# Kernel optimization log

Hardware: AMD Instinct MI355X
Metric: run time of the kernel (lower is better)

## Reference

```python
import jax, jax.numpy as jnp
import numpy as np

NUM_EXPERTS = 8
DIM = 1024
HIDDEN = 2048
N_TOKENS = 8192  # rows of x, includes padding beyond sum(num_tokens_per_expert)


def setup_inputs() -> dict:
    key = jax.random.key(0)
    k_x, k_w1, k_w2, k_w3 = jax.random.split(key, 4)
    x = jax.random.normal(k_x, (N_TOKENS, DIM), dtype=jnp.float32)
    # trunc_normal(std=0.02)-like init; w2 is zeros in torch init but we use
    w1 = jax.random.normal(k_w1, (NUM_EXPERTS, HIDDEN, DIM), dtype=jnp.float32) * 0.02
    w2 = jax.random.normal(k_w2, (NUM_EXPERTS, DIM, HIDDEN), dtype=jnp.float32) * 0.02
    w3 = jax.random.normal(k_w3, (NUM_EXPERTS, HIDDEN, DIM), dtype=jnp.float32) * 0.02
    # routed token counts per expert; sum <= N_TOKENS, remainder is padding
    num_tokens_per_expert = jnp.array([995, 1000, 980, 1010, 970, 1020, 990, 1005], dtype=jnp.int64)
    return {"x": x, "num_tokens_per_expert": num_tokens_per_expert,
            "w1": w1, "w2": w2, "w3": w3}


def reference(x, num_tokens_per_expert, w1, w2, w3):
    # Mirrors torch _run_experts_for_loop with act='silu'. The torch code calls
    # .tolist() on the counts (shapes are data-dependent), so we likewise treat
    # the per-expert counts as static host values.
    counts = np.asarray(num_tokens_per_expert).astype(np.int64)
    offsets = np.concatenate([np.zeros(1, np.int64), np.cumsum(counts)])
    total = int(offsets[-1])
    num_experts = w1.shape[0]
    out_splits = []
    for e in range(num_experts):
        xe = x[int(offsets[e]):int(offsets[e + 1])]            # [n_e, dim]
        gate = jax.nn.silu(xe @ w1[e].T)                       # [n_e, hidden]
        h = gate * (xe @ w3[e].T)                              # SwiGLU
        out_splits.append(h @ w2[e].T)                         # [n_e, dim]
    out = jnp.concatenate(out_splits, axis=0)
    num_padding = x.shape[0] - total
    if num_padding > 0:
        out = jnp.concatenate([out, jnp.zeros((num_padding, out.shape[-1]), out.dtype)], axis=0)
    return out
```

## Files before the change

### kernel.cpp

```cpp
#include <hip/hip_runtime.h>

#define NEXP 8
#define DIM  1024
#define HID  2048
#define NTOK 8192

#define BM 128
#define BN 128
#define BK 32
#define LDK 40
#define CVTY 16

typedef short s16x8 __attribute__((ext_vector_type(8)));
typedef float f32x4 __attribute__((ext_vector_type(4)));
typedef unsigned short u16;

__device__ __forceinline__ u16 f2bf(float f) {
  unsigned int u = __builtin_bit_cast(unsigned int, f);
  u += 0x7FFFu + ((u >> 16) & 1u);
  return (u16)(u >> 16);
}

__device__ __forceinline__ ushort4 cvt4(float4 a) {
  ushort4 r; r.x = f2bf(a.x); r.y = f2bf(a.y); r.z = f2bf(a.z); r.w = f2bf(a.w); return r;
}

__device__ __forceinline__ void gload16(const u16* g, u16* l) {
  __builtin_amdgcn_global_load_lds((const __attribute__((address_space(1))) void*)g,
                                   (__attribute__((address_space(3))) void*)l, 16, 0, 0);
}

__device__ __forceinline__ bool find_tile(const int* __restrict__ cnts, int rt,
                                          int& e_out, int& row0, int& cnt_out, long long& off_out) {
  long long off = 0; int cum = 0;
  #pragma unroll
  for (int e = 0; e < NEXP; ++e) {
    int c = cnts[e];
    int nt = (c + BM - 1) / BM;
    if (rt < cum + nt) { e_out = e; row0 = (rt - cum) * BM; cnt_out = c; off_out = off; return true; }
    cum += nt; off += c;
  }
  return false;
}

__device__ __forceinline__ void cvt32(const float* __restrict__ s, u16* __restrict__ d, int j) {
  const float4* p = (const float4*)s + 8 * (size_t)j;
  float4 a[8];
  #pragma unroll
  for (int q = 0; q < 8; ++q) a[q] = p[q];
  s16x8* dst = (s16x8*)d + 4 * (size_t)j;
  #pragma unroll
  for (int q = 0; q < 4; ++q) {
    s16x8 v;
    v[0] = (short)f2bf(a[2*q].x);   v[1] = (short)f2bf(a[2*q].y);
    v[2] = (short)f2bf(a[2*q].z);   v[3] = (short)f2bf(a[2*q].w);
    v[4] = (short)f2bf(a[2*q+1].x); v[5] = (short)f2bf(a[2*q+1].y);
    v[6] = (short)f2bf(a[2*q+1].z); v[7] = (short)f2bf(a[2*q+1].w);
    dst[q] = v;
  }
}

__global__ __launch_bounds__(256) void cvt_multi(
    const float* __restrict__ s0, u16* __restrict__ d0, int n0,
    const float* __restrict__ s1, u16* __restrict__ d1, int n1,
    const float* __restrict__ s2, u16* __restrict__ d2, int n2,
    const float* __restrict__ s3, u16* __restrict__ d3, int n3) {
  const int b0 = n0, b1 = b0 + n1, b2 = b1 + n2, b3 = b2 + n3;
  for (int i = blockIdx.x * blockDim.x + threadIdx.x; i < b3; i += gridDim.x * blockDim.x) {
    if      (i < b0) cvt32(s0, d0, i);
    else if (i < b1) cvt32(s1, d1, i - b0);
    else if (i < b2) cvt32(s2, d2, i - b1);
    else             cvt32(s3, d3, i - b2);
  }
}

#define XSTR 68
__global__ __launch_bounds__(512, 4) void gemm1_bf16(
    const u16* __restrict__ xb, const int* __restrict__ cnts,
    const u16* __restrict__ w1b, const u16* __restrict__ w3b,
    u16* __restrict__ hbuf,
    const float* __restrict__ w2f, u16* __restrict__ wC, int nW4)
{
  if (blockIdx.y < CVTY) {
    if (nW4) {
      const int cb = blockIdx.y * gridDim.x + blockIdx.x;
      const int T  = CVTY * gridDim.x * 512;
      int i = cb * 512 + threadIdx.x;
      const float4* __restrict__ src = (const float4*)w2f;
      ushort4* __restrict__ dst = (ushort4*)wC;
      for (; i + 3 * T < nW4; i += 4 * T) {
        const float4 a0 = src[i];
        const float4 a1 = src[i + T];
        const float4 a2 = src[i + 2 * T];
        const float4 a3 = src[i + 3 * T];
        dst[i]         = cvt4(a0);
        dst[i + T]     = cvt4(a1);
        dst[i + 2 * T] = cvt4(a2);
        dst[i + 3 * T] = cvt4(a3);
      }
      for (; i < nW4; i += T) dst[i] = cvt4(src[i]);
    }
    return;
  }

  int e, row0, cnt; long long off;
  if (!find_tile(cnts, blockIdx.y - CVTY, e, row0, cnt, off)) return;
  const int ct = blockIdx.x;

  __shared__ __align__(16) u16 smem[3 * 3 * 4096];
  u16* stage = smem;
  float* smem_f = (float*)smem;

  const int t    = threadIdx.x;
  const int lane = t & 63;
  const int wid  = t >> 6;
  const int mat  = wid >> 2;
  const int sw   = wid & 3;
  const int wr = sw >> 1, wc = sw & 1;
  const int lr = lane & 15;
  const int lk = (((lane >> 4) ^ ((lr >> 1) & 3)) << 3);

  const u16* xrow = xb + (size_t)(off + row0) * DIM;
  const u16* w1t  = w1b + ((size_t)e * HID + (size_t)ct * BN) * DIM;
  const u16* w3t  = w3b + ((size_t)e * HID + (size_t)ct * BN) * DIM;

  f32x4 acc[4][4];
  const f32x4 zf = {0.f, 0.f, 0.f, 0.f};
  #pragma unroll
  for (int i = 0; i < 4; ++i)
    #pragma unroll
    for (int j = 0; j < 4; ++j) acc[i][j] = zf;

  const int q    = lane >> 2;
  const int cf   = (lane & 3) ^ ((q >> 1) & 3);
  const int srow = wid * 16 + q;
  const int scol = cf * 8;

  auto STAGE = [&](int k0, int b) {
    u16* base = stage + b * (3 * 4096);
    const size_t go = (size_t)srow * DIM + k0 + scol;
    gload16(&xrow[go], base        + wid * 512);
    gload16(&w1t [go], base + 4096 + wid * 512);
    gload16(&w3t [go], base + 8192 + wid * 512);
  };
  auto COMPUTE = [&](int b) {
    const u16* Asb = stage + b * (3 * 4096);
    const u16* Bsb = Asb + 4096 + mat * 4096;
    s16x8 af[4], bf[4];
    #pragma unroll
    for (int fm = 0; fm < 4; ++fm)
      af[fm] = *(const s16x8*)&Asb[(wr * 64 + fm * 16 + lr) * BK + lk];
    #pragma unroll
    for (int fn = 0; fn < 4; ++fn)
      bf[fn] = *(const s16x8*)&Bsb[(wc * 64 + fn * 16 + lr) * BK + lk];
    __builtin_amdgcn_s_setprio(1);
    #pragma unroll
    for (int fm = 0; fm < 4; ++fm)
      #pragma unroll
      for (int fn = 0; fn < 4; ++fn)
        acc[fm][fn] = __builtin_amdgcn_mfma_f32_16x16x32_bf16(af[fm], bf[fn], acc[fm][fn], 0, 0, 0);
    __builtin_amdgcn_s_setprio(0);
  };

  const int NT = DIM / BK;
  STAGE(0, 0);
  STAGE(BK, 1);
  for (int kt = 0; kt < NT; ++kt) {
    if (kt == NT - 1) { asm volatile("s_waitcnt vmcnt(0)" ::: "memory"); }
    else              { asm volatile("s_waitcnt vmcnt(3)" ::: "memory"); }
    __builtin_amdgcn_s_barrier();
    asm volatile("" ::: "memory");
    if (kt + 2 < NT) STAGE((kt + 2) * BK, (kt + 2) % 3);
    COMPUTE(kt % 3);
  }

  __syncthreads();
  if (mat) {
    float* up = smem_f + sw * (64 * XSTR);
    #pragma unroll
    for (int fm = 0; fm < 4; ++fm)
      #pragma unroll
      for (int fn = 0; fn < 4; ++fn)
        #pragma unroll
        for (int j = 0; j < 4; ++j)
          up[(fm * 16 + ((lane >> 4) << 2) + j) * XSTR + fn * 16 + lr] = acc[fm][fn][j];
  }
  __syncthreads();
  if (!mat) {
    const float* up = smem_f + sw * (64 * XSTR);
    #pragma unroll
    for (int fm = 0; fm < 4; ++fm)
      #pragma unroll
      for (int fn = 0; fn < 4; ++fn) {
        const int col = ct * BN + wc * 64 + fn * 16 + lr;
        #pragma unroll
        for (int j = 0; j < 4; ++j) {
          const int r = wr * 64 + fm * 16 + ((lane >> 4) << 2) + j;
          if (row0 + r < cnt) {
            const float gv = acc[fm][fn][j];
            const float uv = up[(fm * 16 + ((lane >> 4) << 2) + j) * XSTR + fn * 16 + lr];
            const float hv = (gv / (1.f + __expf(-gv))) * uv;
            hbuf[(size_t)(off + row0 + r) * HID + col] = f2bf(hv);
          }
        }
      }
  }
}

__global__ __launch_bounds__(256, 4) void gemm2_bf16(
    const u16* __restrict__ hbuf, const int* __restrict__ cnts,
    const u16* __restrict__ w2b, float* __restrict__ out)
{
  int e, row0, cnt; long long off;
  if (!find_tile(cnts, blockIdx.y, e, row0, cnt, off)) return;
  const int ct = blockIdx.x;

  __shared__ __align__(16) u16 stage[3 * 2 * 4096];

  const int t    = threadIdx.x;
  const int lane = t & 63;
  const int wid  = t >> 6;
  const int wr = wid >> 1, wc = wid & 1;
  const int lr = lane & 15;
  const int lk = (((lane >> 4) ^ ((lr >> 1) & 3)) << 3);

  const u16* arow = hbuf + (size_t)(off + row0) * HID;
  const u16* w2t  = w2b + ((size_t)e * DIM + (size_t)ct * BN) * HID;

  f32x4 acc[4][4];
  const f32x4 zf = {0.f, 0.f, 0.f, 0.f};
  #pragma unroll
  for (int i = 0; i < 4; ++i)
    #pragma unroll
    for (int j = 0; j < 4; ++j) acc[i][j] = zf;

  const int q  = lane >> 2;
  const int cf = (lane & 3) ^ ((q >> 1) & 3);

  auto STAGE = [&](int k0, int b) {
    u16* base = stage + b * (2 * 4096);
    #pragma unroll
    for (int c = 0; c < 2; ++c) {
      const int chunk = wid * 2 + c;
      const int r = chunk * 16 + q;
      const size_t go = (size_t)r * HID + k0 + cf * 8;
      gload16(&arow[go], base        + chunk * 512);
      gload16(&w2t [go], base + 4096 + chunk * 512);
    }
  };
  auto COMPUTE = [&](int b) {
    const u16* Asb = stage + b * (2 * 4096);
    const u16* Bsb = Asb + 4096;
    s16x8 af[4], bf[4];
    #pragma unroll
    for (int fm = 0; fm < 4; ++fm)
      af[fm] = *(const s16x8*)&Asb[(wr * 64 + fm * 16 + lr) * BK + lk];
    #pragma unroll
    for (int fn = 0; fn < 4; ++fn)
      bf[fn] = *(const s16x8*)&Bsb[(wc * 64 + fn * 16 + lr) * BK + lk];
    #pragma unroll
    for (int fm = 0; fm < 4; ++fm)
      #pragma unroll
      for (int fn = 0; fn < 4; ++fn)
        acc[fm][fn] = __builtin_amdgcn_mfma_f32_16x16x32_bf16(af[fm], bf[fn], acc[fm][fn], 0, 0, 0);
  };

  const int NT = HID / BK;
  STAGE(0, 0);
  STAGE(BK, 1);
  for (int kt = 0; kt < NT; ++kt) {
    if (kt == NT - 1) { asm volatile("s_waitcnt vmcnt(0)" ::: "memory"); }
    else              { asm volatile("s_waitcnt vmcnt(4)" ::: "memory"); }
    __builtin_amdgcn_s_barrier();
    asm volatile("" ::: "memory");
    if (kt + 2 < NT) STAGE((kt + 2) * BK, (kt + 2) % 3);
    COMPUTE(kt % 3);
  }

  #pragma unroll
  for (int fm = 0; fm < 4; ++fm)
    #pragma unroll
    for (int fn = 0; fn < 4; ++fn) {
      const int col = ct * BN + wc * 64 + fn * 16 + lr;
      #pragma unroll
      for (int j = 0; j < 4; ++j) {
        const int r = wr * 64 + fm * 16 + ((lane >> 4) << 2) + j;
        if (row0 + r < cnt)
          out[(size_t)(off + row0 + r) * DIM + col] = acc[fm][fn][j];
      }
    }
}

__global__ __launch_bounds__(256) void gemm1_kernel(
    const float* __restrict__ x, const int* __restrict__ cnts,
    const float* __restrict__ w1, const float* __restrict__ w3,
    u16* __restrict__ hbuf)
{
  int e, row0, cnt; long long off;
  if (!find_tile(cnts, blockIdx.y, e, row0, cnt, off)) return;
  const int ct = blockIdx.x;

  __shared__ u16 As [BM * LDK];
  __shared__ u16 B1s[BN * LDK];
  __shared__ u16 B3s[BN * LDK];

  const int t    = threadIdx.x;
  const int srow = t >> 3;
  const int skq  = (t & 7) * 4;
  const int lane = t & 63;
  const int wid  = t >> 6;
  const int wr = wid >> 1, wc = wid & 1;
  const int lr = lane & 15;
  const int lk = (lane >> 4) * 8;

  const float* w1e = w1 + (size_t)e * HID * DIM;
  const float* w3e = w3 + (size_t)e * HID * DIM;

  f32x4 accg[4][4], accu[4][4];
  const f32x4 zf = {0.f, 0.f, 0.f, 0.f};
  #pragma unroll
  for (int i = 0; i < 4; ++i)
    #pragma unroll
    for (int j = 0; j < 4; ++j) { accg[i][j] = zf; accu[i][j] = zf; }

  for (int k0 = 0; k0 < DIM; k0 += BK) {
    __syncthreads();
    #pragma unroll
    for (int s = 0; s < 4; ++s) {
      const int r = s * 32 + srow;
      float4 va = make_float4(0.f, 0.f, 0.f, 0.f);
      const int gm = row0 + r;
      if (gm < cnt) va = *(const float4*)&x[(size_t)(off + gm) * DIM + k0 + skq];
      ushort4 ua; ua.x = f2bf(va.x); ua.y = f2bf(va.y); ua.z = f2bf(va.z); ua.w = f2bf(va.w);
      *(ushort4*)&As[r * LDK + skq] = ua;
      const size_t gb = (size_t)(ct * BN + r) * DIM + k0 + skq;
      const float4 v1 = *(const float4*)&w1e[gb];
      const float4 v3 = *(const float4*)&w3e[gb];
      ushort4 u1; u1.x = f2bf(v1.x); u1.y = f2bf(v1.y); u1.z = f2bf(v1.z); u1.w = f2bf(v1.w);
      ushort4 u3; u3.x = f2bf(v3.x); u3.y = f2bf(v3.y); u3.z = f2bf(v3.z); u3.w = f2bf(v3.w);
      *(ushort4*)&B1s[r * LDK + skq] = u1;
      *(ushort4*)&B3s[r * LDK + skq] = u3;
    }
    __syncthreads();

    s16x8 af[4], b1f[4], b3f[4];
    #pragma unroll
    for (int fm = 0; fm < 4; ++fm)
      af[fm] = *(const s16x8*)&As[(wr * 64 + fm * 16 + lr) * LDK + lk];
    #pragma unroll
    for (int fn = 0; fn < 4; ++fn) {
      b1f[fn] = *(const s16x8*)&B1s[(wc * 64 + fn * 16 + lr) * LDK + lk];
      b3f[fn] = *(const s16x8*)&B3s[(wc * 64 + fn * 16 + lr) * LDK + lk];
    }
    #pragma unroll
    for (int fm = 0; fm < 4; ++fm)
      #pragma unroll
      for (int fn = 0; fn < 4; ++fn) {
        accg[fm][fn] = __builtin_amdgcn_mfma_f32_16x16x32_bf16(af[fm], b1f[fn], accg[fm][fn], 0, 0, 0);
        accu[fm][fn] = __builtin_amdgcn_mfma_f32_16x16x32_bf16(af[fm], b3f[fn], accu[fm][fn], 0, 0, 0);
      }
  }

  #pragma unroll
  for (int fm = 0; fm < 4; ++fm)
    #pragma unroll
    for (int fn = 0; fn < 4; ++fn) {
      const f32x4 g = accg[fm][fn], u = accu[fm][fn];
      const int col = ct * BN + wc * 64 + fn * 16 + lr;
      #pragma unroll
      for (int j = 0; j < 4; ++j) {
        const int r = wr * 64 + fm * 16 + ((lane >> 4) << 2) + j;
        if (row0 + r < cnt) {
          const float gv = g[j];
          const float hv = (gv / (1.f + __expf(-gv))) * u[j];
          hbuf[(size_t)(off + row0 + r) * HID + col] = f2bf(hv);
        }
      }
    }
}

__global__ __launch_bounds__(256) void gemm2_kernel(
    const u16* __restrict__ hbuf, const int* __restrict__ cnts,
    const float* __restrict__ w2, float* __restrict__ out)
{
  int e, row0, cnt; long long off;
  if (!find_tile(cnts, blockIdx.y, e, row0, cnt, off)) return;
  const int ct = blockIdx.x;

  __shared__ u16 As[BM * LDK];
  __shared__ u16 Bs[BN * LDK];

  const int t    = threadIdx.x;
  const int srow = t >> 3;
  const int skq  = (t & 7) * 4;
  const int lane = t & 63;
  const int wid  = t >> 6;
  const int wr = wid >> 1, wc = wid & 1;
  const int lr = lane & 15;
  const int lk = (lane >> 4) * 8;

  const float* w2e = w2 + (size_t)e * DIM * HID;

  f32x4 acc[4][4];
  const f32x4 zf = {0.f, 0.f, 0.f, 0.f};
  #pragma unroll
  for (int i = 0; i < 4; ++i)
    #pragma unroll
    for (int j = 0; j < 4; ++j) acc[i][j] = zf;

  for (int k0 = 0; k0 < HID; k0 += BK) {
    __syncthreads();
    #pragma unroll
    for (int s = 0; s < 4; ++s) {
      const int r = s * 32 + srow;
      ushort4 ua = make_ushort4(0, 0, 0, 0);
      const int gm = row0 + r;
      if (gm < cnt) ua = *(const ushort4*)&hbuf[(size_t)(off + gm) * HID + k0 + skq];
      *(ushort4*)&As[r * LDK + skq] = ua;
      const float4 v2 = *(const float4*)&w2e[(size_t)(ct * BN + r) * HID + k0 + skq];
      ushort4 u2; u2.x = f2bf(v2.x); u2.y = f2bf(v2.y); u2.z = f2bf(v2.z); u2.w = f2bf(v2.w);
      *(ushort4*)&Bs[r * LDK + skq] = u2;
    }
    __syncthreads();

    s16x8 af[4], bf[4];
    #pragma unroll
    for (int fm = 0; fm < 4; ++fm)
      af[fm] = *(const s16x8*)&As[(wr * 64 + fm * 16 + lr) * LDK + lk];
    #pragma unroll
    for (int fn = 0; fn < 4; ++fn)
      bf[fn] = *(const s16x8*)&Bs[(wc * 64 + fn * 16 + lr) * LDK + lk];
    #pragma unroll
    for (int fm = 0; fm < 4; ++fm)
      #pragma unroll
      for (int fn = 0; fn < 4; ++fn)
        acc[fm][fn] = __builtin_amdgcn_mfma_f32_16x16x32_bf16(af[fm], bf[fn], acc[fm][fn], 0, 0, 0);
  }

  #pragma unroll
  for (int fm = 0; fm < 4; ++fm)
    #pragma unroll
    for (int fn = 0; fn < 4; ++fn) {
      const int col = ct * BN + wc * 64 + fn * 16 + lr;
      #pragma unroll
      for (int j = 0; j < 4; ++j) {
        const int r = wr * 64 + fm * 16 + ((lane >> 4) << 2) + j;
        if (row0 + r < cnt)
          out[(size_t)(off + row0 + r) * DIM + col] = acc[fm][fn][j];
      }
    }
}

__global__ void zero_pad_kernel(const int* __restrict__ cnts, float* __restrict__ out)
{
  int total = 0;
  #pragma unroll
  for (int e = 0; e < NEXP; ++e) total += cnts[e];
  for (int row = total + blockIdx.x; row < NTOK; row += gridDim.x) {
    float4* p = (float4*)(out + (size_t)row * DIM);
    p[threadIdx.x] = make_float4(0.f, 0.f, 0.f, 0.f);
  }
}

extern "C" void kernel_launch(void* const* d_in, const int* in_sizes, int n_in,
                              void* d_out, int out_size, void* d_ws, size_t ws_size,
                              hipStream_t stream) {
  const float* x    = (const float*)d_in[0];
  const int*   cnts = (const int*)d_in[1];
  const float* w1   = (const float*)d_in[2];
  const float* w2   = (const float*)d_in[3];
  const float* w3   = (const float*)d_in[4];
  float*       out  = (float*)d_out;

  const size_t HBUF_E = (size_t)NTOK * HID;
  const size_t XB_E   = (size_t)NTOK * DIM;
  const size_t W_E    = (size_t)NEXP * HID * DIM;
  const size_t need_min  = (HBUF_E + XB_E + 2 * W_E) * sizeof(u16);
  const size_t need_full = (HBUF_E + XB_E + 3 * W_E) * sizeof(u16);

  u16* hbuf = (u16*)d_ws;
  dim3 blk(256);
  const int XB32 = (int)(XB_E / 32), W32 = (int)(W_E / 32);
  const int W4   = (int)(W_E / 4);

  if (ws_size >= need_full) {
    u16* xb = hbuf + HBUF_E;
    u16* wA = xb + XB_E;
    u16* wB = wA + W_E;
    u16* wC = wB + W_E;
    cvt_multi<<<dim3(2048), blk, 0, stream>>>(x, xb, XB32, w1, wA, W32, w3, wB, W32,
                                              (const float*)nullptr, (u16*)nullptr, 0);
    gemm1_bf16<<<dim3(HID / BN, 72 + CVTY), dim3(512), 0, stream>>>(xb, cnts, wA, wB, hbuf, w2, wC, W4);
    gemm2_bf16<<<dim3(DIM / BN, 72), blk, 0, stream>>>(hbuf, cnts, wC, out);
  } else if (ws_size >= need_min) {
    u16* xb = hbuf + HBUF_E;
    u16* wA = xb + XB_E;
    u16* wB = wA + W_E;
    cvt_multi<<<dim3(2048), blk, 0, stream>>>(x, xb, XB32, w1, wA, W32, w3, wB, W32,
                                              (const float*)nullptr, (u16*)nullptr, 0);
    gemm1_bf16<<<dim3(HID / BN, 72 + CVTY), dim3(512), 0, stream>>>(xb, cnts, wA, wB, hbuf,
                                                                    (const float*)nullptr, (u16*)nullptr, 0);
    cvt_multi<<<dim3(2048), blk, 0, stream>>>(w2, wA, W32, (const float*)nullptr, (u16*)nullptr, 0,
                                              (const float*)nullptr, (u16*)nullptr, 0,
                                              (const float*)nullptr, (u16*)nullptr, 0);
    gemm2_bf16<<<dim3(DIM / BN, 72), blk, 0, stream>>>(hbuf, cnts, wA, out);
  } else {
    gemm1_kernel<<<dim3(HID / BN, 72), blk, 0, stream>>>(x, cnts, w1, w3, hbuf);
    gemm2_kernel<<<dim3(DIM / BN, 72), blk, 0, stream>>>(hbuf, cnts, w2, out);
  }
  zero_pad_kernel<<<dim3(64), dim3(256), 0, stream>>>(cnts, out);
}
```

Before: 200.8 us.

## Shrink gemm1 tile to 128x64 with 256-thread blocks

Restructures the fused gate/up GEMM from 512-thread blocks computing 128x128 tiles of both w1 and w3 into 256-thread blocks computing 128x64 tiles. Each wave now owns 64 rows against a 64-column slice of one weight matrix. The grid doubles in x, and the CVTY conversion rows are halved to keep the w2 conversion workload balanced. LDS per block drops so more blocks can be resident. The cost is that x tiles are loaded twice as often relative to weights, which lowers arithmetic intensity.

```diff
diff --git a/kernel.cpp b/kernel.cpp
--- a/kernel.cpp
+++ b/kernel.cpp
@@ -9,7 +9,7 @@
 #define BN 128
 #define BK 32
 #define LDK 40
-#define CVTY 16
+#define CVTY 8
 
 typedef short s16x8 __attribute__((ext_vector_type(8)));
 typedef float f32x4 __attribute__((ext_vector_type(4)));
@@ -74,8 +74,7 @@
   }
 }
 
-#define XSTR 68
-__global__ __launch_bounds__(512, 4) void gemm1_bf16(
+__global__ __launch_bounds__(256, 4) void gemm1_bf16(
     const u16* __restrict__ xb, const int* __restrict__ cnts,
     const u16* __restrict__ w1b, const u16* __restrict__ w3b,
     u16* __restrict__ hbuf,
@@ -84,8 +83,8 @@
   if (blockIdx.y < CVTY) {
     if (nW4) {
       const int cb = blockIdx.y * gridDim.x + blockIdx.x;
-      const int T  = CVTY * gridDim.x * 512;
-      int i = cb * 512 + threadIdx.x;
+      const int T  = CVTY * gridDim.x * 256;
+      int i = cb * 256 + threadIdx.x;
       const float4* __restrict__ src = (const float4*)w2f;
       ushort4* __restrict__ dst = (ushort4*)wC;
       for (; i + 3 * T < nW4; i += 4 * T) {
@@ -107,22 +106,21 @@
   if (!find_tile(cnts, blockIdx.y - CVTY, e, row0, cnt, off)) return;
   const int ct = blockIdx.x;
 
-  __shared__ __align__(16) u16 smem[3 * 3 * 4096];
+  __shared__ __align__(16) u16 smem[3 * 8192];
   u16* stage = smem;
   float* smem_f = (float*)smem;
 
   const int t    = threadIdx.x;
   const int lane = t & 63;
   const int wid  = t >> 6;
-  const int mat  = wid >> 2;
-  const int sw   = wid & 3;
-  const int wr = sw >> 1, wc = sw & 1;
-  const int lr = lane & 15;
-  const int lk = (((lane >> 4) ^ ((lr >> 1) & 3)) << 3);
+  const int mat  = wid >> 1;
+  const int sw   = wid & 1;
+  const int lr   = lane & 15;
+  const int lk   = (((lane >> 4) ^ ((lr >> 1) & 3)) << 3);
 
   const u16* xrow = xb + (size_t)(off + row0) * DIM;
-  const u16* w1t  = w1b + ((size_t)e * HID + (size_t)ct * BN) * DIM;
-  const u16* w3t  = w3b + ((size_t)e * HID + (size_t)ct * BN) * DIM;
+  const u16* w1t  = w1b + ((size_t)e * HID + (size_t)ct * 64) * DIM;
+  const u16* w3t  = w3b + ((size_t)e * HID + (size_t)ct * 64) * DIM;
 
   f32x4 acc[4][4];
   const f32x4 zf = {0.f, 0.f, 0.f, 0.f};
@@ -131,28 +129,30 @@
     #pragma unroll
     for (int j = 0; j < 4; ++j) acc[i][j] = zf;
 
-  const int q    = lane >> 2;
-  const int cf   = (lane & 3) ^ ((q >> 1) & 3);
-  const int srow = wid * 16 + q;
+  const int q  = lane >> 2;
+  const int cf = (lane & 3) ^ ((q >> 1) & 3);
   const int scol = cf * 8;
 
   auto STAGE = [&](int k0, int b) {
-    u16* base = stage + b * (3 * 4096);
-    const size_t go = (size_t)srow * DIM + k0 + scol;
-    gload16(&xrow[go], base        + wid * 512);
-    gload16(&w1t [go], base + 4096 + wid * 512);
-    gload16(&w3t [go], base + 8192 + wid * 512);
+    u16* base = stage + b * 8192;
+    const size_t gA0 = (size_t)((wid * 2 + 0) * 16 + q) * DIM + k0 + scol;
+    const size_t gA1 = (size_t)((wid * 2 + 1) * 16 + q) * DIM + k0 + scol;
+    gload16(&xrow[gA0], base + (wid * 2 + 0) * 512);
+    gload16(&xrow[gA1], base + (wid * 2 + 1) * 512);
+    const size_t gB = (size_t)(wid * 16 + q) * DIM + k0 + scol;
+    gload16(&w1t[gB], base + 4096 + wid * 512);
+    gload16(&w3t[gB], base + 6144 + wid * 512);
   };
   auto COMPUTE = [&](int b) {
-    const u16* Asb = stage + b * (3 * 4096);
-    const u16* Bsb = Asb + 4096 + mat * 4096;
+    const u16* Asb = stage + b * 8192;
+    const u16* Bsb = Asb + 4096 + mat * 2048;
     s16x8 af[4], bf[4];
     #pragma unroll
     for (int fm = 0; fm < 4; ++fm)
-      af[fm] = *(const s16x8*)&Asb[(wr * 64 + fm * 16 + lr) * BK + lk];
+      af[fm] = *(const s16x8*)&Asb[(sw * 64 + fm * 16 + lr) * BK + lk];
     #pragma unroll
     for (int fn = 0; fn < 4; ++fn)
-      bf[fn] = *(const s16x8*)&Bsb[(wc * 64 + fn * 16 + lr) * BK + lk];
+      bf[fn] = *(const s16x8*)&Bsb[(fn * 16 + lr) * BK + lk];
     __builtin_amdgcn_s_setprio(1);
     #pragma unroll
     for (int fm = 0; fm < 4; ++fm)
@@ -167,7 +167,7 @@
   STAGE(BK, 1);
   for (int kt = 0; kt < NT; ++kt) {
     if (kt == NT - 1) { asm volatile("s_waitcnt vmcnt(0)" ::: "memory"); }
-    else              { asm volatile("s_waitcnt vmcnt(3)" ::: "memory"); }
+    else              { asm volatile("s_waitcnt vmcnt(4)" ::: "memory"); }
     __builtin_amdgcn_s_barrier();
     asm volatile("" ::: "memory");
     if (kt + 2 < NT) STAGE((kt + 2) * BK, (kt + 2) % 3);
@@ -176,29 +176,29 @@
 
   __syncthreads();
   if (mat) {
-    float* up = smem_f + sw * (64 * XSTR);
+    float* up = smem_f + sw * (64 * 68);
     #pragma unroll
     for (int fm = 0; fm < 4; ++fm)
       #pragma unroll
       for (int fn = 0; fn < 4; ++fn)
         #pragma unroll
         for (int j = 0; j < 4; ++j)
-          up[(fm * 16 + ((lane >> 4) << 2) + j) * XSTR + fn * 16 + lr] = acc[fm][fn][j];
+          up[(fm * 16 + ((lane >> 4) << 2) + j) * 68 + fn * 16 + lr] = acc[fm][fn][j];
   }
   __syncthreads();
   if (!mat) {
-    const float* up = smem_f + sw * (64 * XSTR);
+    const float* up = smem_f + sw * (64 * 68);
     #pragma unroll
     for (int fm = 0; fm < 4; ++fm)
       #pragma unroll
       for (int fn = 0; fn < 4; ++fn) {
-        const int col = ct * BN + wc * 64 + fn * 16 + lr;
+        const int col = ct * 64 + fn * 16 + lr;
         #pragma unroll
         for (int j = 0; j < 4; ++j) {
-          const int r = wr * 64 + fm * 16 + ((lane >> 4) << 2) + j;
+          const int r = sw * 64 + fm * 16 + ((lane >> 4) << 2) + j;
           if (row0 + r < cnt) {
             const float gv = acc[fm][fn][j];
-            const float uv = up[(fm * 16 + ((lane >> 4) << 2) + j) * XSTR + fn * 16 + lr];
+            const float uv = up[(fm * 16 + ((lane >> 4) << 2) + j) * 68 + fn * 16 + lr];
             const float hv = (gv / (1.f + __expf(-gv))) * uv;
             hbuf[(size_t)(off + row0 + r) * HID + col] = f2bf(hv);
           }
@@ -490,7 +490,7 @@
     u16* wC = wB + W_E;
     cvt_multi<<<dim3(2048), blk, 0, stream>>>(x, xb, XB32, w1, wA, W32, w3, wB, W32,
                                               (const float*)nullptr, (u16*)nullptr, 0);
-    gemm1_bf16<<<dim3(HID / BN, 72 + CVTY), dim3(512), 0, stream>>>(xb, cnts, wA, wB, hbuf, w2, wC, W4);
+    gemm1_bf16<<<dim3(HID / 64, 72 + CVTY), blk, 0, stream>>>(xb, cnts, wA, wB, hbuf, w2, wC, W4);
     gemm2_bf16<<<dim3(DIM / BN, 72), blk, 0, stream>>>(hbuf, cnts, wC, out);
   } else if (ws_size >= need_min) {
     u16* xb = hbuf + HBUF_E;
@@ -498,8 +498,8 @@
     u16* wB = wA + W_E;
     cvt_multi<<<dim3(2048), blk, 0, stream>>>(x, xb, XB32, w1, wA, W32, w3, wB, W32,
                                               (const float*)nullptr, (u16*)nullptr, 0);
-    gemm1_bf16<<<dim3(HID / BN, 72 + CVTY), dim3(512), 0, stream>>>(xb, cnts, wA, wB, hbuf,
-                                                                    (const float*)nullptr, (u16*)nullptr, 0);
+    gemm1_bf16<<<dim3(HID / 64, 72 + CVTY), blk, 0, stream>>>(xb, cnts, wA, wB, hbuf,
+                                                              (const float*)nullptr, (u16*)nullptr, 0);
     cvt_multi<<<dim3(2048), blk, 0, stream>>>(w2, wA, W32, (const float*)nullptr, (u16*)nullptr, 0,
                                               (const float*)nullptr, (u16*)nullptr, 0,
                                               (const float*)nullptr, (u16*)nullptr, 0);
```

After: 219.0 us. 1.09x slower.
